# Performance work log

Hardware: AMD Instinct MI355X
Metric: run time of the kernel (lower is better)

## Reference

```python
import jax, jax.numpy as jnp
import numpy as np

D_MODEL = 1024
NUM_HEADS = 16
HEAD_DIM = D_MODEL // NUM_HEADS
BATCH = 2
SEQ = 2048


def setup_inputs() -> dict:
    key = jax.random.key(0)
    ks = jax.random.split(key, 9)
    s = 1.0 / np.sqrt(D_MODEL)
    inp = {
        "x": jax.random.normal(ks[0], (BATCH, SEQ, D_MODEL), dtype=jnp.float32),
        "mask": jnp.ones((BATCH, SEQ), dtype=jnp.int32),
        "Wq": jax.random.uniform(ks[1], (D_MODEL, D_MODEL), jnp.float32, -s, s),
        "bq": jax.random.uniform(ks[2], (D_MODEL,), jnp.float32, -s, s),
        "Wk": jax.random.uniform(ks[3], (D_MODEL, D_MODEL), jnp.float32, -s, s),
        "bk": jax.random.uniform(ks[4], (D_MODEL,), jnp.float32, -s, s),
        "Wv": jax.random.uniform(ks[5], (D_MODEL, D_MODEL), jnp.float32, -s, s),
        "bv": jax.random.uniform(ks[6], (D_MODEL,), jnp.float32, -s, s),
        "Wo": jax.random.uniform(ks[7], (D_MODEL, D_MODEL), jnp.float32, -s, s),
        "bo": jax.random.uniform(ks[8], (D_MODEL,), jnp.float32, -s, s),
    }
    return inp


def reference(x, mask, Wq, bq, Wk, bk, Wv, bv, Wo, bo):
    B, S, D = x.shape
    H, Hd = NUM_HEADS, HEAD_DIM
    # torch Linear: y = x @ W.T + b ; then reshape to [B, H, S, Hd]
    def proj(W, b):
        return (x @ W.T + b).reshape(B, S, H, Hd).transpose(0, 2, 1, 3)
    Q = proj(Wq, bq)
    K = proj(Wk, bk)
    V = proj(Wv, bv)
    scale = 1.0 / jnp.sqrt(jnp.asarray(Hd, dtype=x.dtype))
    scores = jnp.einsum("bhqd,bhkd->bhqk", Q, K) * scale  # [B,H,S,S]
    # mask [B,S] -> broadcast over query positions; masked_fill(mask==0, -1e9)
    scores = jnp.where(mask[:, None, None, :] == 0, jnp.asarray(-1e9, x.dtype), scores)
    attn = jax.nn.softmax(scores, axis=-1)
    context = jnp.einsum("bhqk,bhkd->bhqd", attn, V)
    context = context.transpose(0, 2, 1, 3).reshape(B, S, D)
    return context @ Wo.T + bo
```

## Files before the change

kernel.cpp:

```cpp
#include <hip/hip_runtime.h>
#include <hip/hip_bf16.h>
#include <cstdint>

#define D_MODEL 1024
#define NUM_HEADS 16
#define HEAD_DIM 64
#define BATCH 2
#define SEQ 2048
#define MROWS (BATCH * SEQ)

typedef __attribute__((ext_vector_type(8))) short bf16x8;
typedef __attribute__((ext_vector_type(4))) float f32x4;
typedef unsigned short u16;

#define QSCALE (0.125f * 1.44269504f)

#if __has_builtin(__builtin_amdgcn_exp2f)
#define EXP2F(x) __builtin_amdgcn_exp2f(x)
#else
#define EXP2F(x) exp2f(x)
#endif

static __device__ __forceinline__ u16 f2bf(float f) {
    unsigned int u = __float_as_uint(f);
    unsigned int lsb = (u >> 16) & 1u;
    u += 0x7fffu + lsb;
    return (u16)(u >> 16);
}

#if __has_builtin(__builtin_amdgcn_cvt_pk_bf16_f32)
static __device__ __forceinline__ unsigned pkbf(float a, float b) {
    typedef __attribute__((ext_vector_type(2))) __bf16 bf2;
    union { bf2 v; unsigned u; } cv;
    cv.v = __builtin_amdgcn_cvt_pk_bf16_f32(a, b);
    return cv.u;
}
#else
static __device__ __forceinline__ unsigned pkbf(float a, float b) {
    unsigned ua = (__float_as_uint(a) + 0x8000u) >> 16;
    unsigned ub = (__float_as_uint(b) + 0x8000u) & 0xffff0000u;
    return ua | ub;
}
#endif

static __device__ __forceinline__ void gload_lds16(const void* g, void* l) {
    __builtin_amdgcn_global_load_lds((const __attribute__((address_space(1))) unsigned int*)g,
                                     (__attribute__((address_space(3))) unsigned int*)l,
                                     16, 0, 0);
}

__global__ void cvt_bf16(const float* __restrict__ src,
                         u16* __restrict__ dst, int n) {
    int i = (blockIdx.x * blockDim.x + threadIdx.x) * 4;
    if (i + 3 < n) {
        float4 v = *(const float4*)(src + i);
        ushort4 o;
        o.x = f2bf(v.x); o.y = f2bf(v.y); o.z = f2bf(v.z); o.w = f2bf(v.w);
        *(ushort4*)(dst + i) = o;
    }
}

__global__ void cvt_bf16_4(const float* __restrict__ s0, const float* __restrict__ s1,
                           const float* __restrict__ s2, const float* __restrict__ s3,
                           u16* __restrict__ dst, int n_each) {
    const int which = blockIdx.y;
    const float* s = (which == 0) ? s0 : (which == 1) ? s1 : (which == 2) ? s2 : s3;
    int i = (blockIdx.x * blockDim.x + threadIdx.x) * 4;
    if (i + 3 < n_each) {
        float4 v = *(const float4*)(s + i);
        ushort4 o;
        o.x = f2bf(v.x); o.y = f2bf(v.y); o.z = f2bf(v.z); o.w = f2bf(v.w);
        *(ushort4*)(dst + (size_t)which * n_each + i) = o;
    }
}

template<int BN, int MODE>
__global__ __launch_bounds__(256, 3)
void gemm_staged(const u16* __restrict__ A, const u16* __restrict__ W,
                 const float* __restrict__ b0, const float* __restrict__ b1,
                 const float* __restrict__ b2,
                 u16* __restrict__ o0, u16* __restrict__ o1, u16* __restrict__ o2,
                 float* __restrict__ of, int K, int N) {
    constexpr int WN = BN / 2;
    constexpr int NJ = WN / 16;
    __shared__ __align__(16) u16 As[128 * 64];
    __shared__ __align__(16) u16 Bs[BN * 64];

    const int lane = threadIdx.x & 63;
    const int w    = threadIdx.x >> 6;
    const int quad = lane >> 4;
    const int l16  = lane & 15;
    const int wm = w >> 1, wn = w & 1;

    const u16* Ablk = A + (size_t)(blockIdx.y * 128) * K;
    const u16* Wblk = W + (size_t)(blockIdx.x * BN) * K;

    const int srow = lane >> 3;
    const int scol = lane & 7;

    f32x4 acc[4][NJ];
#pragma unroll
    for (int i = 0; i < 4; ++i)
#pragma unroll
        for (int j = 0; j < NJ; ++j) acc[i][j] = (f32x4){0.f, 0.f, 0.f, 0.f};

    for (int kb0 = 0; kb0 < K; kb0 += 64) {
        __syncthreads();
#pragma unroll
        for (int t = 0; t < 4; ++t) {
            const int r  = w * 32 + t * 8 + srow;
            const int cg = scol ^ (r & 7);
            gload_lds16(Ablk + (size_t)r * K + kb0 + cg * 8, &As[(w * 32 + t * 8) * 64]);
        }
#pragma unroll
        for (int t = 0; t < BN / 32; ++t) {
            const int r  = w * (BN / 4) + t * 8 + srow;
            const int cg = scol ^ (r & 7);
            gload_lds16(Wblk + (size_t)r * K + kb0 + cg * 8, &Bs[(w * (BN / 4) + t * 8) * 64]);
        }
        __syncthreads();
#pragma unroll
        for (int ks = 0; ks < 2; ++ks) {
            bf16x8 a[4], b[NJ];
#pragma unroll
            for (int i = 0; i < 4; ++i) {
                const int ra = wm * 64 + 16 * i + l16;
                a[i] = *(const bf16x8*)&As[ra * 64 + ((ks * 4 + quad) ^ (ra & 7)) * 8];
            }
#pragma unroll
            for (int j = 0; j < NJ; ++j) {
                const int rb = wn * WN + 16 * j + l16;
                b[j] = *(const bf16x8*)&Bs[rb * 64 + ((ks * 4 + quad) ^ (rb & 7)) * 8];
            }
#pragma unroll
            for (int i = 0; i < 4; ++i)
#pragma unroll
                for (int j = 0; j < NJ; ++j)
                    acc[i][j] = __builtin_amdgcn_mfma_f32_16x16x32_bf16(a[i], b[j], acc[i][j], 0, 0, 0);
        }
    }

    const int mbase = blockIdx.y * 128 + wm * 64;
    const int nbase = blockIdx.x * BN + wn * WN;

    if (MODE == 0) {
#pragma unroll
        for (int j = 0; j < NJ; ++j) {
            const int gn = nbase + 16 * j + l16;
            const int which = gn >> 10, rem = gn & 1023;
            const float bv = (which == 0 ? b0 : which == 1 ? b1 : b2)[rem];
            u16* dst = (which == 0) ? o0 : (which == 1) ? o1 : o2;
            const float scl = (which == 0) ? QSCALE : 1.0f;
            const int h = rem >> 6, d = rem & 63;
#pragma unroll
            for (int i = 0; i < 4; ++i)
#pragma unroll
                for (int r = 0; r < 4; ++r) {
                    const int gm = mbase + 16 * i + quad * 4 + r;
                    const int bb = gm >> 11, s = gm & 2047;
                    dst[(((size_t)(bb * NUM_HEADS + h) * SEQ) + s) * 64 + d] =
                        f2bf((acc[i][j][r] + bv) * scl);
                }
        }
    } else {
#pragma unroll
        for (int j = 0; j < NJ; ++j) {
            const int gn = nbase + 16 * j + l16;
            const float bv = b0[gn];
#pragma unroll
            for (int i = 0; i < 4; ++i)
#pragma unroll
                for (int r = 0; r < 4; ++r) {
                    const int gm = mbase + 16 * i + quad * 4 + r;
                    of[(size_t)gm * N + gn] = acc[i][j][r] + bv;
                }
        }
    }
}

__global__ void transpose_v(const u16* __restrict__ V, u16* __restrict__ VT) {
    __shared__ __align__(16) u16 T[64 * 64];
    const int t    = threadIdx.x;
    const int lane = t & 63, w = t >> 6;
    const int bh   = blockIdx.x & 31, sblk = blockIdx.x >> 5;
    const u16* src = V + ((size_t)bh * SEQ + sblk * 64) * 64;

#pragma unroll
    for (int p = 0; p < 2; ++p) {
        const int r = p * 32 + w * 8 + (lane >> 3);
        const int c = lane & 7;
        bf16x8 v = *(const bf16x8*)(src + r * 64 + c * 8);
        *(bf16x8*)&T[r * 64 + ((c ^ (r & 7)) * 8)] = v;
    }
    __syncthreads();
    u16* dst = VT + ((size_t)bh * 64) * SEQ + sblk * 64;
#pragma unroll
    for (int p = 0; p < 2; ++p) {
        const int r  = p * 32 + w * 8 + (lane >> 3);
        const int sc = lane & 7;
        union { u16 u[8]; bf16x8 v; } pk;
#pragma unroll
        for (int j = 0; j < 8; ++j)
            pk.u[j] = T[(sc * 8 + j) * 64 + (((r >> 3) ^ j) * 8) + (r & 7)];
        *(bf16x8*)(dst + (size_t)r * SEQ + sc * 8) = pk.v;
    }
}

__global__ __launch_bounds__(256, 2)
void attn_kernel(const u16* __restrict__ Q, const u16* __restrict__ K,
                 const u16* __restrict__ VT, const int* __restrict__ mask,
                 u16* __restrict__ ctx) {
    __shared__ __align__(16) u16 Ks[2][64 * 64];
    __shared__ __align__(16) u16 Vs[2][64 * 64];
    __shared__ __align__(16) u16 Ps[4][32 * 72];

    const int lane = threadIdx.x & 63;
    const int w    = threadIdx.x >> 6;
    const int quad = lane >> 4;
    const int l16  = lane & 15;

    const int bh = blockIdx.x & 31;
    const int qb = blockIdx.x >> 5;
    const int b  = bh >> 4;
    const int h  = bh & 15;
    const int qbase = qb * 128 + w * 32;

    const u16* Qh = Q + (size_t)bh * SEQ * 64;
    const u16* Kh = K + (size_t)bh * SEQ * 64;
    const u16* Vh = VT + (size_t)bh * 64 * SEQ;
    const int* mrow = mask + b * SEQ;

    const int srow = lane >> 3;
    const int scol = lane & 7;

#pragma unroll
    for (int t = 0; t < 2; ++t) {
        const int r  = 16 * w + 8 * t + srow;
        const int cg = scol ^ (r & 7);
        gload_lds16(Kh + (size_t)r * 64 + cg * 8, &Ks[0][(16 * w + 8 * t) * 64]);
        gload_lds16(Vh + (size_t)r * SEQ + cg * 8, &Vs[0][(16 * w + 8 * t) * 64]);
    }

    bf16x8 qf[2][2];
#pragma unroll
    for (int iq = 0; iq < 2; ++iq)
#pragma unroll
        for (int ks = 0; ks < 2; ++ks)
            qf[iq][ks] = *(const bf16x8*)(Qh + (size_t)(qbase + 16 * iq + l16) * 64 + 32 * ks + quad * 8);

    f32x4 o[2][4];
#pragma unroll
    for (int iq = 0; iq < 2; ++iq)
#pragma unroll
        for (int id = 0; id < 4; ++id) o[iq][id] = (f32x4){0.f, 0.f, 0.f, 0.f};
    float lst[2] = {0.f, 0.f};

    unsigned short* myp = &Ps[w][0];
    const int rowsel = (lane & 48) | (quad * 4);

    for (int kb = 0; kb < 32; ++kb) {
        const int cur = kb & 1;
        __syncthreads();

        if (kb != 31) {
            const int kn = (kb + 1) * 64;
#pragma unroll
            for (int t = 0; t < 2; ++t) {
                const int r  = 16 * w + 8 * t + srow;
                const int cg = scol ^ (r & 7);
                gload_lds16(Kh + (size_t)(kn + r) * 64 + cg * 8, &Ks[cur ^ 1][(16 * w + 8 * t) * 64]);
                gload_lds16(Vh + (size_t)r * SEQ + kn + cg * 8, &Vs[cur ^ 1][(16 * w + 8 * t) * 64]);
            }
        }

        const int kstart = kb * 64;
        const int mv = mrow[kstart + lane];
        const bool clean = (__ballot(mv != 0) == ~0ull);

        bf16x8 kf[4][2];
#pragma unroll
        for (int ik = 0; ik < 4; ++ik) {
            const int row = 16 * ik + l16;
#pragma unroll
            for (int ks = 0; ks < 2; ++ks)
                kf[ik][ks] = *(const bf16x8*)&Ks[cur][row * 64 + ((4 * ks + quad) ^ (row & 7)) * 8];
        }

        f32x4 s[4][2];
#pragma unroll
        for (int ik = 0; ik < 4; ++ik)
#pragma unroll
            for (int iq = 0; iq < 2; ++iq) {
                f32x4 t = (f32x4){0.f, 0.f, 0.f, 0.f};
                t = __builtin_amdgcn_mfma_f32_16x16x32_bf16(kf[ik][0], qf[iq][0], t, 0, 0, 0);
                t = __builtin_amdgcn_mfma_f32_16x16x32_bf16(kf[ik][1], qf[iq][1], t, 0, 0, 0);
                s[ik][iq] = t;
            }

        bf16x8 vf[4][2];
#pragma unroll
        for (int id = 0; id < 4; ++id) {
            const int row = 16 * id + l16;
#pragma unroll
            for (int ks = 0; ks < 2; ++ks)
                vf[id][ks] = *(const bf16x8*)&Vs[cur][row * 64 + ((4 * ks + quad) ^ (row & 7)) * 8];
        }

        if (!clean) {
            int4 mk[4];
#pragma unroll
            for (int ik = 0; ik < 4; ++ik)
                mk[ik] = *(const int4*)(mrow + kstart + 16 * ik + quad * 4);
#pragma unroll
            for (int ik = 0; ik < 4; ++ik) {
                const int* mp = (const int*)&mk[ik];
#pragma unroll
                for (int r = 0; r < 4; ++r) {
                    const bool keep = (mp[r] != 0);
#pragma unroll
                    for (int iq = 0; iq < 2; ++iq)
                        s[ik][iq][r] = keep ? s[ik][iq][r] : -1e9f;
                }
            }
        }

#pragma unroll
        for (int iq = 0; iq < 2; ++iq) {
            float rs = 0.f;
#pragma unroll
            for (int ik = 0; ik < 4; ++ik) {
                const float p0 = EXP2F(fminf(s[ik][iq][0], 80.f));
                const float p1 = EXP2F(fminf(s[ik][iq][1], 80.f));
                const float p2 = EXP2F(fminf(s[ik][iq][2], 80.f));
                const float p3 = EXP2F(fminf(s[ik][iq][3], 80.f));
                rs += (p0 + p1) + (p2 + p3);
                uint2 pk;
                pk.x = pkbf(p0, p1);
                pk.y = pkbf(p2, p3);
                *(uint2*)(myp + (16 * iq + l16) * 72 + 16 * ik + quad * 4) = pk;
            }
            rs += __shfl_xor(rs, 16, 64);
            rs += __shfl_xor(rs, 32, 64);
            lst[iq] += rs;
        }

#pragma unroll
        for (int ks = 0; ks < 2; ++ks) {
            bf16x8 pf[2];
#pragma unroll
            for (int iq = 0; iq < 2; ++iq)
                pf[iq] = *(const bf16x8*)(myp + (16 * iq + l16) * 72 + 32 * ks + quad * 8);
#pragma unroll
            for (int iq = 0; iq < 2; ++iq)
#pragma unroll
                for (int id = 0; id < 4; ++id)
                    o[iq][id] = __builtin_amdgcn_mfma_f32_16x16x32_bf16(pf[iq], vf[id][ks], o[iq][id], 0, 0, 0);
        }
    }

#pragma unroll
    for (int iq = 0; iq < 2; ++iq) {
        float linv[4];
#pragma unroll
        for (int r = 0; r < 4; ++r) linv[r] = 1.f / __shfl(lst[iq], rowsel + r, 64);
#pragma unroll
        for (int id = 0; id < 4; ++id)
#pragma unroll
            for (int r = 0; r < 4; ++r) {
                const int q = qbase + 16 * iq + quad * 4 + r;
                const int d = 16 * id + l16;
                ctx[((size_t)(b * SEQ + q)) * D_MODEL + h * 64 + d] = f2bf(o[iq][id][r] * linv[r]);
            }
    }
}

extern "C" void kernel_launch(void* const* d_in, const int* in_sizes, int n_in,
                              void* d_out, int out_size, void* d_ws, size_t ws_size,
                              hipStream_t stream) {
    const float* x    = (const float*)d_in[0];
    const int*   mask = (const int*)d_in[1];
    const float* Wq   = (const float*)d_in[2];
    const float* bq   = (const float*)d_in[3];
    const float* Wk   = (const float*)d_in[4];
    const float* bk   = (const float*)d_in[5];
    const float* Wv   = (const float*)d_in[6];
    const float* bv   = (const float*)d_in[7];
    const float* Wo   = (const float*)d_in[8];
    const float* bo   = (const float*)d_in[9];

    u16* xb  = (u16*)d_ws;
    u16* wqb = xb  + (size_t)MROWS * D_MODEL;
    u16* wkb = wqb + (size_t)D_MODEL * D_MODEL;
    u16* wvb = wkb + (size_t)D_MODEL * D_MODEL;
    u16* wob = wvb + (size_t)D_MODEL * D_MODEL;
    u16* Qb  = wob + (size_t)D_MODEL * D_MODEL;
    u16* Kb  = Qb  + (size_t)MROWS * D_MODEL;
    u16* VTb = Kb  + (size_t)MROWS * D_MODEL;
    u16* ctx = VTb + (size_t)MROWS * D_MODEL;

    const int nx = MROWS * D_MODEL;
    const int nw = D_MODEL * D_MODEL;
    cvt_bf16<<<nx / 1024, 256, 0, stream>>>(x, xb, nx);
    cvt_bf16_4<<<dim3(nw / 1024, 4), 256, 0, stream>>>(Wq, Wk, Wv, Wo, wqb, nw);

    gemm_staged<128, 0><<<dim3(3 * D_MODEL / 128, MROWS / 128), 256, 0, stream>>>(
        xb, wqb, bq, bk, bv, Qb, Kb, ctx, nullptr, D_MODEL, 3 * D_MODEL);

    transpose_v<<<BATCH * NUM_HEADS * (SEQ / 64), 256, 0, stream>>>(ctx, VTb);

    attn_kernel<<<BATCH * NUM_HEADS * (SEQ / 128), 256, 0, stream>>>(Qb, Kb, VTb, mask, ctx);

    gemm_staged<64, 1><<<dim3(D_MODEL / 64, MROWS / 128), 256, 0, stream>>>(
        ctx, wob, bo, nullptr, nullptr, nullptr, nullptr, nullptr,
        (float*)d_out, D_MODEL, D_MODEL);
}
```

Baseline: 212.9 us.

## Split attention work across 8 waves of 16 query rows each

The attention kernel now launches 512 threads per block, with each wave owning 16 query rows instead of 32. K/V tile loads are split across 8 waves with one load each. Fewer registers per wave should allow more waves per CU, giving better latency hiding. The trade-off is that each K/V fragment read from LDS now feeds half as many MFMAs, so LDS traffic per FLOP doubles.

```diff
diff --git a/kernel.cpp b/kernel.cpp
--- a/kernel.cpp
+++ b/kernel.cpp
@@ -206,13 +206,13 @@
     }
 }
 
-__global__ __launch_bounds__(256, 2)
+__global__ __launch_bounds__(512, 4)
 void attn_kernel(const u16* __restrict__ Q, const u16* __restrict__ K,
                  const u16* __restrict__ VT, const int* __restrict__ mask,
                  u16* __restrict__ ctx) {
     __shared__ __align__(16) u16 Ks[2][64 * 64];
     __shared__ __align__(16) u16 Vs[2][64 * 64];
-    __shared__ __align__(16) u16 Ps[4][32 * 72];
+    __shared__ __align__(16) u16 Ps[8][16 * 72];
 
     const int lane = threadIdx.x & 63;
     const int w    = threadIdx.x >> 6;
@@ -223,7 +223,7 @@
     const int qb = blockIdx.x >> 5;
     const int b  = bh >> 4;
     const int h  = bh & 15;
-    const int qbase = qb * 128 + w * 32;
+    const int qbase = qb * 128 + w * 16;
 
     const u16* Qh = Q + (size_t)bh * SEQ * 64;
     const u16* Kh = K + (size_t)bh * SEQ * 64;
@@ -232,45 +232,35 @@
 
     const int srow = lane >> 3;
     const int scol = lane & 7;
-
-#pragma unroll
-    for (int t = 0; t < 2; ++t) {
-        const int r  = 16 * w + 8 * t + srow;
-        const int cg = scol ^ (r & 7);
-        gload_lds16(Kh + (size_t)r * 64 + cg * 8, &Ks[0][(16 * w + 8 * t) * 64]);
-        gload_lds16(Vh + (size_t)r * SEQ + cg * 8, &Vs[0][(16 * w + 8 * t) * 64]);
-    }
-
-    bf16x8 qf[2][2];
-#pragma unroll
-    for (int iq = 0; iq < 2; ++iq)
-#pragma unroll
-        for (int ks = 0; ks < 2; ++ks)
-            qf[iq][ks] = *(const bf16x8*)(Qh + (size_t)(qbase + 16 * iq + l16) * 64 + 32 * ks + quad * 8);
-
-    f32x4 o[2][4];
-#pragma unroll
-    for (int iq = 0; iq < 2; ++iq)
-#pragma unroll
-        for (int id = 0; id < 4; ++id) o[iq][id] = (f32x4){0.f, 0.f, 0.f, 0.f};
-    float lst[2] = {0.f, 0.f};
+    const int cg   = scol ^ srow;
+
+    gload_lds16(Kh + (size_t)(8 * w + srow) * 64 + cg * 8, &Ks[0][(8 * w) * 64]);
+    gload_lds16(Vh + (size_t)(8 * w + srow) * SEQ + cg * 8, &Vs[0][(8 * w) * 64]);
+
+    bf16x8 qf[2];
+#pragma unroll
+    for (int ks = 0; ks < 2; ++ks)
+        qf[ks] = *(const bf16x8*)(Qh + (size_t)(qbase + l16) * 64 + 32 * ks + quad * 8);
+
+    f32x4 o[4];
+#pragma unroll
+    for (int id = 0; id < 4; ++id) o[id] = (f32x4){0.f, 0.f, 0.f, 0.f};
+    float lst = 0.f;
 
     unsigned short* myp = &Ps[w][0];
     const int rowsel = (lane & 48) | (quad * 4);
 
+#pragma unroll 2
     for (int kb = 0; kb < 32; ++kb) {
         const int cur = kb & 1;
         __syncthreads();
 
         if (kb != 31) {
             const int kn = (kb + 1) * 64;
-#pragma unroll
-            for (int t = 0; t < 2; ++t) {
-                const int r  = 16 * w + 8 * t + srow;
-                const int cg = scol ^ (r & 7);
-                gload_lds16(Kh + (size_t)(kn + r) * 64 + cg * 8, &Ks[cur ^ 1][(16 * w + 8 * t) * 64]);
-                gload_lds16(Vh + (size_t)r * SEQ + kn + cg * 8, &Vs[cur ^ 1][(16 * w + 8 * t) * 64]);
-            }
+            gload_lds16(Kh + (size_t)(kn + 8 * w + srow) * 64 + cg * 8,
+                        &Ks[cur ^ 1][(8 * w) * 64]);
+            gload_lds16(Vh + (size_t)(8 * w + srow) * SEQ + kn + cg * 8,
+                        &Vs[cur ^ 1][(8 * w) * 64]);
         }
 
         const int kstart = kb * 64;
@@ -286,16 +276,14 @@
                 kf[ik][ks] = *(const bf16x8*)&Ks[cur][row * 64 + ((4 * ks + quad) ^ (row & 7)) * 8];
         }
 
-        f32x4 s[4][2];
-#pragma unroll
-        for (int ik = 0; ik < 4; ++ik)
-#pragma unroll
-            for (int iq = 0; iq < 2; ++iq) {
-                f32x4 t = (f32x4){0.f, 0.f, 0.f, 0.f};
-                t = __builtin_amdgcn_mfma_f32_16x16x32_bf16(kf[ik][0], qf[iq][0], t, 0, 0, 0);
-                t = __builtin_amdgcn_mfma_f32_16x16x32_bf16(kf[ik][1], qf[iq][1], t, 0, 0, 0);
-                s[ik][iq] = t;
-            }
+        f32x4 s[4];
+#pragma unroll
+        for (int ik = 0; ik < 4; ++ik) {
+            f32x4 t = (f32x4){0.f, 0.f, 0.f, 0.f};
+            t = __builtin_amdgcn_mfma_f32_16x16x32_bf16(kf[ik][0], qf[0], t, 0, 0, 0);
+            t = __builtin_amdgcn_mfma_f32_16x16x32_bf16(kf[ik][1], qf[1], t, 0, 0, 0);
+            s[ik] = t;
+        }
 
         bf16x8 vf[4][2];
 #pragma unroll
@@ -307,71 +295,53 @@
         }
 
         if (!clean) {
-            int4 mk[4];
-#pragma unroll
-            for (int ik = 0; ik < 4; ++ik)
-                mk[ik] = *(const int4*)(mrow + kstart + 16 * ik + quad * 4);
 #pragma unroll
             for (int ik = 0; ik < 4; ++ik) {
-                const int* mp = (const int*)&mk[ik];
-#pragma unroll
-                for (int r = 0; r < 4; ++r) {
-                    const bool keep = (mp[r] != 0);
-#pragma unroll
-                    for (int iq = 0; iq < 2; ++iq)
-                        s[ik][iq][r] = keep ? s[ik][iq][r] : -1e9f;
-                }
+                int4 mk = *(const int4*)(mrow + kstart + 16 * ik + quad * 4);
+                const int* mp = (const int*)&mk;
+#pragma unroll
+                for (int r = 0; r < 4; ++r)
+                    s[ik][r] = (mp[r] != 0) ? s[ik][r] : -1e9f;
             }
         }
 
-#pragma unroll
-        for (int iq = 0; iq < 2; ++iq) {
-            float rs = 0.f;
-#pragma unroll
-            for (int ik = 0; ik < 4; ++ik) {
-                const float p0 = EXP2F(fminf(s[ik][iq][0], 80.f));
-                const float p1 = EXP2F(fminf(s[ik][iq][1], 80.f));
-                const float p2 = EXP2F(fminf(s[ik][iq][2], 80.f));
-                const float p3 = EXP2F(fminf(s[ik][iq][3], 80.f));
-                rs += (p0 + p1) + (p2 + p3);
-                uint2 pk;
-                pk.x = pkbf(p0, p1);
-                pk.y = pkbf(p2, p3);
-                *(uint2*)(myp + (16 * iq + l16) * 72 + 16 * ik + quad * 4) = pk;
-            }
-            rs += __shfl_xor(rs, 16, 64);
-            rs += __shfl_xor(rs, 32, 64);
-            lst[iq] += rs;
-        }
+        float rs = 0.f;
+#pragma unroll
+        for (int ik = 0; ik < 4; ++ik) {
+            const float p0 = EXP2F(fminf(s[ik][0], 80.f));
+            const float p1 = EXP2F(fminf(s[ik][1], 80.f));
+            const float p2 = EXP2F(fminf(s[ik][2], 80.f));
+            const float p3 = EXP2F(fminf(s[ik][3], 80.f));
+            rs += (p0 + p1) + (p2 + p3);
+            uint2 pk;
+            pk.x = pkbf(p0, p1);
+            pk.y = pkbf(p2, p3);
+            *(uint2*)(myp + l16 * 72 + 16 * ik + quad * 4) = pk;
+        }
+        rs += __shfl_xor(rs, 16, 64);
+        rs += __shfl_xor(rs, 32, 64);
+        lst += rs;
 
 #pragma unroll
         for (int ks = 0; ks < 2; ++ks) {
-            bf16x8 pf[2];
-#pragma unroll
-            for (int iq = 0; iq < 2; ++iq)
-                pf[iq] = *(const bf16x8*)(myp + (16 * iq + l16) * 72 + 32 * ks + quad * 8);
-#pragma unroll
-            for (int iq = 0; iq < 2; ++iq)
-#pragma unroll
-                for (int id = 0; id < 4; ++id)
-                    o[iq][id] = __builtin_amdgcn_mfma_f32_16x16x32_bf16(pf[iq], vf[id][ks], o[iq][id], 0, 0, 0);
-        }
-    }
-
-#pragma unroll
-    for (int iq = 0; iq < 2; ++iq) {
-        float linv[4];
-#pragma unroll
-        for (int r = 0; r < 4; ++r) linv[r] = 1.f / __shfl(lst[iq], rowsel + r, 64);
-#pragma unroll
-        for (int id = 0; id < 4; ++id)
-#pragma unroll
-            for (int r = 0; r < 4; ++r) {
-                const int q = qbase + 16 * iq + quad * 4 + r;
-                const int d = 16 * id + l16;
-                ctx[((size_t)(b * SEQ + q)) * D_MODEL + h * 64 + d] = f2bf(o[iq][id][r] * linv[r]);
-            }
-    }
+            bf16x8 pf = *(const bf16x8*)(myp + l16 * 72 + 32 * ks + quad * 8);
+#pragma unroll
+            for (int id = 0; id < 4; ++id)
+                o[id] = __builtin_amdgcn_mfma_f32_16x16x32_bf16(pf, vf[id][ks], o[id], 0, 0, 0);
+        }
+    }
+
+    float linv[4];
+#pragma unroll
+    for (int r = 0; r < 4; ++r) linv[r] = 1.f / __shfl(lst, rowsel + r, 64);
+#pragma unroll
+    for (int id = 0; id < 4; ++id)
+#pragma unroll
+        for (int r = 0; r < 4; ++r) {
+            const int q = qbase + quad * 4 + r;
+            const int d = 16 * id + l16;
+            ctx[((size_t)(b * SEQ + q)) * D_MODEL + h * 64 + d] = f2bf(o[id][r] * linv[r]);
+        }
 }
 
 extern "C" void kernel_launch(void* const* d_in, const int* in_sizes, int n_in,
@@ -408,7 +378,7 @@
 
     transpose_v<<<BATCH * NUM_HEADS * (SEQ / 64), 256, 0, stream>>>(ctx, VTb);
 
-    attn_kernel<<<BATCH * NUM_HEADS * (SEQ / 128), 256, 0, stream>>>(Qb, Kb, VTb, mask, ctx);
+    attn_kernel<<<BATCH * NUM_HEADS * (SEQ / 128), 512, 0, stream>>>(Qb, Kb, VTb, mask, ctx);
 
     gemm_staged<64, 1><<<dim3(D_MODEL / 64, MROWS / 128), 256, 0, stream>>>(
         ctx, wob, bo, nullptr, nullptr, nullptr, nullptr, nullptr,
```

Result: faster. 203.6 us (-4.4%).

## Merge conversions into one launch and double attention block to 8 waves

Applied to the files above, without the earlier changes.

The two fp32-to-bf16 conversion kernels become a single launch that handles x and all four weight matrices through an 8-slice grid, saving one kernel launch. The attention kernel now runs 512 threads (8 waves) per block covering 256 queries, so each K/V tile loaded into LDS is shared by twice as many query rows and each wave issues half as many async loads. The KV loop is unrolled by two and the mask reads are moved into the loop. In exchange the grid has half as many blocks (256), which may underfill the GPU and lengthen barrier waits across 8 waves.

```diff
diff --git a/kernel.cpp b/kernel.cpp
--- a/kernel.cpp
+++ b/kernel.cpp
@@ -49,29 +49,24 @@
                                      16, 0, 0);
 }
 
-__global__ void cvt_bf16(const float* __restrict__ src,
-                         u16* __restrict__ dst, int n) {
-    int i = (blockIdx.x * blockDim.x + threadIdx.x) * 4;
-    if (i + 3 < n) {
-        float4 v = *(const float4*)(src + i);
-        ushort4 o;
-        o.x = f2bf(v.x); o.y = f2bf(v.y); o.z = f2bf(v.z); o.w = f2bf(v.w);
-        *(ushort4*)(dst + i) = o;
-    }
-}
-
-__global__ void cvt_bf16_4(const float* __restrict__ s0, const float* __restrict__ s1,
-                           const float* __restrict__ s2, const float* __restrict__ s3,
-                           u16* __restrict__ dst, int n_each) {
+__global__ void cvt_all(const float* __restrict__ x,
+                        const float* __restrict__ w0, const float* __restrict__ w1,
+                        const float* __restrict__ w2, const float* __restrict__ w3,
+                        u16* __restrict__ base) {
     const int which = blockIdx.y;
-    const float* s = (which == 0) ? s0 : (which == 1) ? s1 : (which == 2) ? s2 : s3;
-    int i = (blockIdx.x * blockDim.x + threadIdx.x) * 4;
-    if (i + 3 < n_each) {
-        float4 v = *(const float4*)(s + i);
-        ushort4 o;
-        o.x = f2bf(v.x); o.y = f2bf(v.y); o.z = f2bf(v.z); o.w = f2bf(v.w);
-        *(ushort4*)(dst + (size_t)which * n_each + i) = o;
-    }
+    const int NE = D_MODEL * D_MODEL;
+    const float* s;
+    if (which < 4)      s = x + (size_t)which * NE;
+    else if (which == 4) s = w0;
+    else if (which == 5) s = w1;
+    else if (which == 6) s = w2;
+    else                 s = w3;
+    u16* dst = base + (size_t)which * NE;
+    const int i = (blockIdx.x * blockDim.x + threadIdx.x) * 4;
+    float4 v = *(const float4*)(s + i);
+    ushort4 o;
+    o.x = f2bf(v.x); o.y = f2bf(v.y); o.z = f2bf(v.z); o.w = f2bf(v.w);
+    *(ushort4*)(dst + i) = o;
 }
 
 template<int BN, int MODE>
@@ -206,13 +201,13 @@
     }
 }
 
-__global__ __launch_bounds__(256, 2)
+__global__ __launch_bounds__(512, 2)
 void attn_kernel(const u16* __restrict__ Q, const u16* __restrict__ K,
                  const u16* __restrict__ VT, const int* __restrict__ mask,
                  u16* __restrict__ ctx) {
     __shared__ __align__(16) u16 Ks[2][64 * 64];
     __shared__ __align__(16) u16 Vs[2][64 * 64];
-    __shared__ __align__(16) u16 Ps[4][32 * 72];
+    __shared__ __align__(16) u16 Ps[8][32 * 72];
 
     const int lane = threadIdx.x & 63;
     const int w    = threadIdx.x >> 6;
@@ -223,7 +218,7 @@
     const int qb = blockIdx.x >> 5;
     const int b  = bh >> 4;
     const int h  = bh & 15;
-    const int qbase = qb * 128 + w * 32;
+    const int qbase = qb * 256 + w * 32;
 
     const u16* Qh = Q + (size_t)bh * SEQ * 64;
     const u16* Kh = K + (size_t)bh * SEQ * 64;
@@ -232,14 +227,10 @@
 
     const int srow = lane >> 3;
     const int scol = lane & 7;
-
-#pragma unroll
-    for (int t = 0; t < 2; ++t) {
-        const int r  = 16 * w + 8 * t + srow;
-        const int cg = scol ^ (r & 7);
-        gload_lds16(Kh + (size_t)r * 64 + cg * 8, &Ks[0][(16 * w + 8 * t) * 64]);
-        gload_lds16(Vh + (size_t)r * SEQ + cg * 8, &Vs[0][(16 * w + 8 * t) * 64]);
-    }
+    const int cg   = scol ^ srow;
+
+    gload_lds16(Kh + (size_t)(8 * w + srow) * 64 + cg * 8, &Ks[0][(8 * w) * 64]);
+    gload_lds16(Vh + (size_t)(8 * w + srow) * SEQ + cg * 8, &Vs[0][(8 * w) * 64]);
 
     bf16x8 qf[2][2];
 #pragma unroll
@@ -258,19 +249,17 @@
     unsigned short* myp = &Ps[w][0];
     const int rowsel = (lane & 48) | (quad * 4);
 
+#pragma unroll 2
     for (int kb = 0; kb < 32; ++kb) {
         const int cur = kb & 1;
         __syncthreads();
 
         if (kb != 31) {
             const int kn = (kb + 1) * 64;
-#pragma unroll
-            for (int t = 0; t < 2; ++t) {
-                const int r  = 16 * w + 8 * t + srow;
-                const int cg = scol ^ (r & 7);
-                gload_lds16(Kh + (size_t)(kn + r) * 64 + cg * 8, &Ks[cur ^ 1][(16 * w + 8 * t) * 64]);
-                gload_lds16(Vh + (size_t)r * SEQ + kn + cg * 8, &Vs[cur ^ 1][(16 * w + 8 * t) * 64]);
-            }
+            gload_lds16(Kh + (size_t)(kn + 8 * w + srow) * 64 + cg * 8,
+                        &Ks[cur ^ 1][(8 * w) * 64]);
+            gload_lds16(Vh + (size_t)(8 * w + srow) * SEQ + kn + cg * 8,
+                        &Vs[cur ^ 1][(8 * w) * 64]);
         }
 
         const int kstart = kb * 64;
@@ -307,13 +296,10 @@
         }
 
         if (!clean) {
-            int4 mk[4];
-#pragma unroll
-            for (int ik = 0; ik < 4; ++ik)
-                mk[ik] = *(const int4*)(mrow + kstart + 16 * ik + quad * 4);
 #pragma unroll
             for (int ik = 0; ik < 4; ++ik) {
-                const int* mp = (const int*)&mk[ik];
+                int4 mk = *(const int4*)(mrow + kstart + 16 * ik + quad * 4);
+                const int* mp = (const int*)&mk;
 #pragma unroll
                 for (int r = 0; r < 4; ++r) {
                     const bool keep = (mp[r] != 0);
@@ -390,25 +376,21 @@
 
     u16* xb  = (u16*)d_ws;
     u16* wqb = xb  + (size_t)MROWS * D_MODEL;
-    u16* wkb = wqb + (size_t)D_MODEL * D_MODEL;
-    u16* wvb = wkb + (size_t)D_MODEL * D_MODEL;
-    u16* wob = wvb + (size_t)D_MODEL * D_MODEL;
+    u16* wob = wqb + (size_t)3 * D_MODEL * D_MODEL;
     u16* Qb  = wob + (size_t)D_MODEL * D_MODEL;
     u16* Kb  = Qb  + (size_t)MROWS * D_MODEL;
     u16* VTb = Kb  + (size_t)MROWS * D_MODEL;
     u16* ctx = VTb + (size_t)MROWS * D_MODEL;
 
-    const int nx = MROWS * D_MODEL;
-    const int nw = D_MODEL * D_MODEL;
-    cvt_bf16<<<nx / 1024, 256, 0, stream>>>(x, xb, nx);
-    cvt_bf16_4<<<dim3(nw / 1024, 4), 256, 0, stream>>>(Wq, Wk, Wv, Wo, wqb, nw);
+    cvt_all<<<dim3(D_MODEL * D_MODEL / 1024, 8), 256, 0, stream>>>(
+        x, Wq, Wk, Wv, Wo, xb);
 
     gemm_staged<128, 0><<<dim3(3 * D_MODEL / 128, MROWS / 128), 256, 0, stream>>>(
         xb, wqb, bq, bk, bv, Qb, Kb, ctx, nullptr, D_MODEL, 3 * D_MODEL);
 
     transpose_v<<<BATCH * NUM_HEADS * (SEQ / 64), 256, 0, stream>>>(ctx, VTb);
 
-    attn_kernel<<<BATCH * NUM_HEADS * (SEQ / 128), 256, 0, stream>>>(Qb, Kb, VTb, mask, ctx);
+    attn_kernel<<<BATCH * NUM_HEADS * (SEQ / 256), 512, 0, stream>>>(Qb, Kb, VTb, mask, ctx);
 
     gemm_staged<64, 1><<<dim3(D_MODEL / 64, MROWS / 128), 256, 0, stream>>>(
         ctx, wob, bo, nullptr, nullptr, nullptr, nullptr, nullptr,
```

Result: faster. 203.7 us (-4.3%).
